# Kernel optimization log

Hardware: AMD Instinct MI355X
Metric: run time of the kernel (lower is better)

Reference implementation:

```python
import jax, jax.numpy as jnp
import numpy as np

EPS = 1e-5

# Binary activation with straight-through estimator (custom backward in the
# original torch.autograd.Function: grad scaled by 0.01 where |x| >= 1).
@jax.custom_vjp
def binact(x):
    return jnp.sign(x)

def _binact_fwd(x):
    return jnp.sign(x), x

def _binact_bwd(x, g):
    return (jnp.where((x >= 1.0) | (x <= -1.0), g * 0.01, g),)

binact.defvjp(_binact_fwd, _binact_bwd)


def batchnorm(x, gamma, beta):
    # training-mode BN: biased batch stats over (N, H, W)
    m = jnp.mean(x, axis=(0, 2, 3), keepdims=True)
    v = jnp.var(x, axis=(0, 2, 3), keepdims=True)
    return (x - m) * jax.lax.rsqrt(v + EPS) * gamma[None, :, None, None] + beta[None, :, None, None]


def prelu(x, alpha):
    return jnp.where(x >= 0, x, alpha[None, :, None, None] * x)


def binconv(x, w, stride):
    # per-output-channel scaling factor = mean |w| over (in, kh, kw), detached
    sf = jax.lax.stop_gradient(jnp.mean(jnp.abs(w), axis=(1, 2, 3), keepdims=True))
    bw = sf * jnp.sign(w)                       # binarized weight (+-sf)
    rc = jnp.clip(w, -1.0, 1.0)                 # STE path for gradients
    bf = jax.lax.stop_gradient(bw - rc) + rc    # forward=bw, backward=d(clip)
    return jax.lax.conv_general_dilated(
        x, bf, window_strides=(stride, stride), padding=[(1, 1), (1, 1)],
        dimension_numbers=("NCHW", "OIHW", "NCHW"))


def setup_inputs() -> dict:
    key = jax.random.key(0)
    ks = jax.random.split(key, 3)
    B, Cin, Cp, H = 32, 256, 256, 56
    x = jax.random.normal(ks[0], (B, Cin, H, H), jnp.float32)
    # original init: torch.rand(...) * 0.001; centered here so sign() has both polarities
    w1 = (jax.random.uniform(ks[1], (Cp, Cin, 3, 3), jnp.float32) * 2.0 - 1.0) * 0.001
    w2 = (jax.random.uniform(ks[2], (Cp, Cp, 3, 3), jnp.float32) * 2.0 - 1.0) * 0.001
    return {
        "x": x, "w1": w1, "w2": w2,
        "g1": jnp.ones((Cin,), jnp.float32), "b1": jnp.zeros((Cin,), jnp.float32),
        "g2": jnp.ones((Cp,), jnp.float32), "b2": jnp.zeros((Cp,), jnp.float32),
        "g3": jnp.ones((Cp,), jnp.float32), "b3": jnp.zeros((Cp,), jnp.float32),
        "a1": jnp.full((Cp,), 0.25, jnp.float32),
        "a2": jnp.full((Cp,), 0.25, jnp.float32),
        "a3": jnp.full((Cp,), 0.25, jnp.float32),
    }


def reference(x, w1, w2, g1, b1, g2, b2, g3, b3, a1, a2, a3):
    out = batchnorm(x, g1, b1)
    out = binact(out)
    out = prelu(binconv(out, w1, 1), a1)
    out = batchnorm(out, g2, b2)
    out = binact(out)
    out = binconv(out, w2, 1)
    out = prelu(out, a2)
    out = batchnorm(out, g3, b3)
    out = out + x  # identity shortcut (stride=1, in_planes == planes)
    return prelu(out, a3)
```

## Files before the change

kernel.cpp:

```cpp
#include <hip/hip_runtime.h>
#include <hip/hip_bf16.h>

typedef short short8 __attribute__((ext_vector_type(8)));
typedef float f32x4 __attribute__((ext_vector_type(4)));

#define NB 32
#define NC 256
#define HW 56
#define HALO 58
#define NPIX 100352
#define PIXB 3136

__device__ inline void gl_lds16(const void* g, void* l) {
    __builtin_amdgcn_global_load_lds(
        (const __attribute__((address_space(1))) void*)g,
        (__attribute__((address_space(3))) void*)l, 16, 0, 0);
}

__device__ inline unsigned short sgn_bf16(float v) {
    return v > 0.f ? (unsigned short)0x3F80 : (v < 0.f ? (unsigned short)0xBF80 : (unsigned short)0);
}

__global__ void halo_zero(unsigned short* __restrict__ s) {
    const uint4 z = {0u, 0u, 0u, 0u};
    const int total = 32 * 228 * 32;
    for (int v = blockIdx.x * 256 + threadIdx.x; v < total; v += gridDim.x * 256) {
        int cellg = v >> 5, q = v & 31;
        int b = cellg / 228;
        int cell = cellg - b * 228;
        int y, xx;
        if (cell < 58)       { y = 0;          xx = cell; }
        else if (cell < 116) { y = 57;         xx = cell - 58; }
        else if (cell < 172) { y = cell - 115; xx = 0; }
        else                 { y = cell - 171; xx = 57; }
        *(uint4*)(s + (((size_t)b * HALO + y) * HALO + xx) * 256 + q * 8) = z;
    }
}

__global__ void wprep_kernel(const float* __restrict__ w, unsigned short* __restrict__ wsgn,
                             float* __restrict__ sf) {
    int oc = blockIdx.x;
    const float* wp = w + (size_t)oc * 2304;
    unsigned short* op = wsgn + (size_t)oc * 2304;
    float s = 0.f;
    for (int idx = threadIdx.x; idx < 2304; idx += 256) {
        float v = wp[idx];
        s += fabsf(v);
        int ic = idx / 9;
        int k = idx - ic * 9;
        op[k * 256 + ic] = sgn_bf16(v);
    }
    #pragma unroll
    for (int m = 32; m; m >>= 1) s += __shfl_xor(s, m);
    __shared__ float rs[4];
    if ((threadIdx.x & 63) == 0) rs[threadIdx.x >> 6] = s;
    __syncthreads();
    if (threadIdx.x == 0) sf[oc] = (rs[0] + rs[1] + rs[2] + rs[3]) * (1.f / 2304.f);
}

__global__ void bn_stats_x(const float* __restrict__ x, double* __restrict__ ssum,
                           double* __restrict__ ssq) {
    int bid = blockIdx.x;
    int c = bid >> 3;
    int bg = bid & 7;
    float s = 0.f, q = 0.f;
    for (int b = bg * 4; b < bg * 4 + 4; ++b) {
        const float4* p = (const float4*)(x + ((size_t)(b * 256 + c)) * PIXB);
        for (int u = threadIdx.x; u < 784; u += 256) {
            float4 v = p[u];
            s += v.x + v.y + v.z + v.w;
            q += v.x * v.x + v.y * v.y + v.z * v.z + v.w * v.w;
        }
    }
    #pragma unroll
    for (int m = 32; m; m >>= 1) { s += __shfl_xor(s, m); q += __shfl_xor(q, m); }
    __shared__ float rs[4], rq[4];
    if ((threadIdx.x & 63) == 0) { rs[threadIdx.x >> 6] = s; rq[threadIdx.x >> 6] = q; }
    __syncthreads();
    if (threadIdx.x == 0) {
        atomicAdd(&ssum[c], (double)(rs[0] + rs[1] + rs[2] + rs[3]));
        atomicAdd(&ssq[c], (double)(rq[0] + rq[1] + rq[2] + rq[3]));
    }
}

__global__ void bn_finalize(const double* __restrict__ ssum, const double* __restrict__ ssq,
                            const float* __restrict__ g, const float* __restrict__ b,
                            float* __restrict__ scale, float* __restrict__ shift) {
    int c = threadIdx.x;
    double m = ssum[c] * (1.0 / (double)NPIX);
    double v = ssq[c] * (1.0 / (double)NPIX) - m * m;
    double sc = (double)g[c] / sqrt(v + 1e-5);
    scale[c] = (float)sc;
    shift[c] = (float)((double)b[c] - m * sc);
}

__global__ void sign1_kernel(const float* __restrict__ x, const float* __restrict__ scale,
                             const float* __restrict__ shift, unsigned short* __restrict__ sdst) {
    __shared__ unsigned short lds[64 * 57];
    int bid = blockIdx.x;
    int b = bid / 224;
    int rem = bid - b * 224;
    int h = rem >> 2;
    int cg = rem & 3;
    for (int idx = threadIdx.x; idx < 896; idx += 256) {
        int cl = idx / 14;
        int w4 = idx - cl * 14;
        int c = cg * 64 + cl;
        float4 v = *(const float4*)(x + ((((size_t)b * 256 + c) * 56 + h) * 56) + w4 * 4);
        float sc = scale[c], sh = shift[c];
        lds[cl * 57 + w4 * 4 + 0] = sgn_bf16(v.x * sc + sh);
        lds[cl * 57 + w4 * 4 + 1] = sgn_bf16(v.y * sc + sh);
        lds[cl * 57 + w4 * 4 + 2] = sgn_bf16(v.z * sc + sh);
        lds[cl * 57 + w4 * 4 + 3] = sgn_bf16(v.w * sc + sh);
    }
    __syncthreads();
    unsigned short* dst = sdst + (((size_t)b * HALO + h + 1) * HALO + 1) * 256 + cg * 64;
    for (int u = threadIdx.x; u < 896; u += 256) {
        int w = u >> 4;
        int c4 = u & 15;
        ushort4 o;
        o.x = lds[(c4 * 4 + 0) * 57 + w];
        o.y = lds[(c4 * 4 + 1) * 57 + w];
        o.z = lds[(c4 * 4 + 2) * 57 + w];
        o.w = lds[(c4 * 4 + 3) * 57 + w];
        *(ushort4*)(dst + w * 256 + c4 * 4) = o;
    }
}

__global__ void sign2_kernel(const float* __restrict__ y, const float* __restrict__ scale,
                             const float* __restrict__ shift, unsigned short* __restrict__ sdst) {
    int bid = blockIdx.x;
    int b = bid / 56;
    int h = bid - b * 56;
    const float4* src = (const float4*)(y + (size_t)bid * 56 * 256);
    unsigned short* dst = sdst + (((size_t)b * HALO + h + 1) * HALO + 1) * 256;
    for (int u = threadIdx.x; u < 3584; u += 256) {
        int c0 = (u & 63) * 4;
        float4 v = src[u];
        float4 sc = *(const float4*)(scale + c0);
        float4 sh = *(const float4*)(shift + c0);
        ushort4 o;
        o.x = sgn_bf16(v.x * sc.x + sh.x);
        o.y = sgn_bf16(v.y * sc.y + sh.y);
        o.z = sgn_bf16(v.z * sc.z + sh.z);
        o.w = sgn_bf16(v.w * sc.w + sh.w);
        *(ushort4*)(dst + (size_t)u * 4) = o;
    }
}

__global__ void conv_kernel(const unsigned short* __restrict__ sact,
                            const unsigned short* __restrict__ wsgn,
                            const float* __restrict__ sf, const float* __restrict__ alpha,
                            float* __restrict__ y, double* __restrict__ stat_sum,
                            double* __restrict__ stat_sumsq) {
    __shared__ char smem[16384];
    char* ldsA = smem;
    char* ldsB = smem + 8192;

    const int tid = threadIdx.x;
    const int lane = tid & 63;
    const int wave = tid >> 6;
    const int wm = wave >> 1, wn = wave & 1;

    const int bid = blockIdx.x;
    const int oc0 = (bid & 1) * 128;
    const int pix0 = (bid >> 1) * 128;

    const char* sBytes = (const char*)sact;
    const char* wBytes = (const char*)wsgn;
    int aBase[2], bBase[2];
    #pragma unroll
    for (int j = 0; j < 2; ++j) {
        int pix = pix0 + j * 64 + lane;
        int b = pix / PIXB;
        int rem = pix - b * PIXB;
        int oh = rem / 56;
        int ow = rem - oh * 56;
        aBase[j] = ((b * HALO + oh) * HALO + ow) * 512;
        bBase[j] = (oc0 + j * 64 + lane) * 4608;
    }

    f32x4 acc[4][4];
    #pragma unroll
    for (int m = 0; m < 4; ++m)
        #pragma unroll
        for (int n = 0; n < 4; ++n) acc[m][n] = {0.f, 0.f, 0.f, 0.f};

    const int fi = lane & 15;
    const int fc = lane >> 4;
    const int aOffBase = fc * 2048 + (wm * 64 + fi) * 16;
    const int bOffBase = fc * 2048 + (wn * 64 + fi) * 16;
    char* ldsA_st = ldsA + wave * 2048;
    char* ldsB_st = ldsB + wave * 2048;
    const int kSt = wave * 16;

    #pragma unroll 1
    for (int tap = 0; tap < 9; ++tap) {
        const int tapOff = ((tap / 3) * HALO + (tap % 3)) * 512;
        const int wTap = tap * 512;
        #pragma unroll
        for (int sl = 0; sl < 8; ++sl) {
            const int aoff = tapOff + sl * 64 + kSt;
            const int woff = wTap + sl * 64 + kSt;
            gl_lds16(sBytes + aBase[0] + aoff, ldsA_st);
            gl_lds16(sBytes + aBase[1] + aoff, ldsA_st + 1024);
            gl_lds16(wBytes + bBase[0] + woff, ldsB_st);
            gl_lds16(wBytes + bBase[1] + woff, ldsB_st + 1024);
            __syncthreads();
            short8 af[4], bf[4];
            #pragma unroll
            for (int m = 0; m < 4; ++m) af[m] = *(const short8*)(ldsA + aOffBase + m * 256);
            #pragma unroll
            for (int n = 0; n < 4; ++n) bf[n] = *(const short8*)(ldsB + bOffBase + n * 256);
            #pragma unroll
            for (int m = 0; m < 4; ++m)
                #pragma unroll
                for (int n = 0; n < 4; ++n)
                    acc[m][n] = __builtin_amdgcn_mfma_f32_16x16x32_bf16(af[m], bf[n], acc[m][n], 0, 0, 0);
            __syncthreads();
        }
    }

    float sfv[4], alv[4];
    #pragma unroll
    for (int n = 0; n < 4; ++n) {
        int oc = oc0 + wn * 64 + n * 16 + fi;
        sfv[n] = sf[oc];
        alv[n] = alpha[oc];
    }

    float* trans = (float*)smem;
    float* redS = (float*)(smem + 8192);
    float* redQ = (float*)(smem + 12288);
    const int cg = tid & 31;
    const int prw = tid >> 5;
    float ts[4] = {0.f, 0.f, 0.f, 0.f}, tq[4] = {0.f, 0.f, 0.f, 0.f};

    #pragma unroll
    for (int seg = 0; seg < 8; ++seg) {
        const int swm = seg >> 2, smi = seg & 3;
        if (wm == swm) {
            #pragma unroll
            for (int n = 0; n < 4; ++n) {
                f32x4 v = acc[smi][n];
                #pragma unroll
                for (int r = 0; r < 4; ++r) {
                    float val = v[r] * sfv[n];
                    val = val >= 0.f ? val : val * alv[n];
                    trans[(fc * 4 + r) * 128 + wn * 64 + n * 16 + fi] = val;
                }
            }
        }
        __syncthreads();
        #pragma unroll
        for (int i = 0; i < 2; ++i) {
            int p = prw + i * 8;
            f32x4 v = *(f32x4*)&trans[p * 128 + cg * 4];
            *(f32x4*)(y + (size_t)(pix0 + seg * 16 + p) * 256 + oc0 + cg * 4) = v;
            #pragma unroll
            for (int j = 0; j < 4; ++j) { ts[j] += v[j]; tq[j] += v[j] * v[j]; }
        }
        __syncthreads();
    }

    #pragma unroll
    for (int j = 0; j < 4; ++j) {
        redS[prw * 128 + cg * 4 + j] = ts[j];
        redQ[prw * 128 + cg * 4 + j] = tq[j];
    }
    __syncthreads();
    if (tid < 128) {
        float s = 0.f, q = 0.f;
        #pragma unroll
        for (int r = 0; r < 8; ++r) { s += redS[r * 128 + tid]; q += redQ[r * 128 + tid]; }
        atomicAdd(&stat_sum[oc0 + tid], (double)s);
        atomicAdd(&stat_sumsq[oc0 + tid], (double)q);
    }
}

__global__ void final_kernel(const float* __restrict__ z, const float* __restrict__ x,
                             const float* __restrict__ scale, const float* __restrict__ shift,
                             const float* __restrict__ a3, float* __restrict__ out) {
    __shared__ float lds[56 * 65];
    int bid = blockIdx.x;
    int b = bid / 224;
    int rem = bid - b * 224;
    int h = rem >> 2;
    int cg = rem & 3;
    for (int u = threadIdx.x; u < 896; u += 256) {
        int w = u >> 4;
        int c4 = u & 15;
        float4 v = *(const float4*)(z + ((size_t)(b * PIXB + h * 56 + w)) * 256 + cg * 64 + c4 * 4);
        int c = cg * 64 + c4 * 4;
        lds[w * 65 + c4 * 4 + 0] = v.x * scale[c + 0] + shift[c + 0];
        lds[w * 65 + c4 * 4 + 1] = v.y * scale[c + 1] + shift[c + 1];
        lds[w * 65 + c4 * 4 + 2] = v.z * scale[c + 2] + shift[c + 2];
        lds[w * 65 + c4 * 4 + 3] = v.w * scale[c + 3] + shift[c + 3];
    }
    __syncthreads();
    for (int u = threadIdx.x; u < 896; u += 256) {
        int cl = u / 14;
        int w4 = u - cl * 14;
        int c = cg * 64 + cl;
        size_t off = ((((size_t)b * 256 + c) * 56 + h) * 56) + w4 * 4;
        float4 xv = *(const float4*)(x + off);
        float av = a3[c];
        float4 o;
        o.x = lds[(w4 * 4 + 0) * 65 + cl] + xv.x;
        o.y = lds[(w4 * 4 + 1) * 65 + cl] + xv.y;
        o.z = lds[(w4 * 4 + 2) * 65 + cl] + xv.z;
        o.w = lds[(w4 * 4 + 3) * 65 + cl] + xv.w;
        o.x = o.x >= 0.f ? o.x : o.x * av;
        o.y = o.y >= 0.f ? o.y : o.y * av;
        o.z = o.z >= 0.f ? o.z : o.z * av;
        o.w = o.w >= 0.f ? o.w : o.w * av;
        *(float4*)(out + off) = o;
    }
}

extern "C" void kernel_launch(void* const* d_in, const int* in_sizes, int n_in,
                              void* d_out, int out_size, void* d_ws, size_t ws_size,
                              hipStream_t stream) {
    const float* x = (const float*)d_in[0];
    const float* w1 = (const float*)d_in[1];
    const float* w2 = (const float*)d_in[2];
    const float* g1 = (const float*)d_in[3];
    const float* b1 = (const float*)d_in[4];
    const float* g2 = (const float*)d_in[5];
    const float* b2 = (const float*)d_in[6];
    const float* g3 = (const float*)d_in[7];
    const float* b3 = (const float*)d_in[8];
    const float* a1 = (const float*)d_in[9];
    const float* a2 = (const float*)d_in[10];
    const float* a3 = (const float*)d_in[11];
    float* out = (float*)d_out;

    char* ws = (char*)d_ws;
    size_t off = 0;
    auto alloc = [&](size_t bytes) {
        char* p = ws + off;
        off += (bytes + 255) & ~(size_t)255;
        return p;
    };
    const size_t SBUF_BYTES = (size_t)NB * HALO * HALO * 256 * 2;
    unsigned short* s_buf = (unsigned short*)alloc(SBUF_BYTES);
    float* y_buf = (float*)alloc((size_t)NPIX * 256 * 4);
    unsigned short* wsg1 = (unsigned short*)alloc(256 * 2304 * 2);
    unsigned short* wsg2 = (unsigned short*)alloc(256 * 2304 * 2);
    float* sf1 = (float*)alloc(1024);
    float* sf2 = (float*)alloc(1024);
    double* stats = (double*)alloc(6 * 256 * 8);
    float* scales = (float*)alloc(6 * 256 * 4);

    double *sum1 = stats, *q1 = stats + 256, *sum2 = stats + 512, *q2 = stats + 768,
           *sum3 = stats + 1024, *q3 = stats + 1280;
    float *scale1 = scales, *shift1 = scales + 256, *scale2 = scales + 512,
          *shift2 = scales + 768, *scale3 = scales + 1024, *shift3 = scales + 1280;

    hipMemsetAsync(stats, 0, 6 * 256 * 8, stream);

    halo_zero<<<256, 256, 0, stream>>>(s_buf);
    wprep_kernel<<<256, 256, 0, stream>>>(w1, wsg1, sf1);
    wprep_kernel<<<256, 256, 0, stream>>>(w2, wsg2, sf2);
    bn_stats_x<<<2048, 256, 0, stream>>>(x, sum1, q1);
    bn_finalize<<<1, 256, 0, stream>>>(sum1, q1, g1, b1, scale1, shift1);
    sign1_kernel<<<7168, 256, 0, stream>>>(x, scale1, shift1, s_buf);
    conv_kernel<<<1568, 256, 0, stream>>>(s_buf, wsg1, sf1, a1, y_buf, sum2, q2);
    bn_finalize<<<1, 256, 0, stream>>>(sum2, q2, g2, b2, scale2, shift2);
    sign2_kernel<<<1792, 256, 0, stream>>>(y_buf, scale2, shift2, s_buf);
    conv_kernel<<<1568, 256, 0, stream>>>(s_buf, wsg2, sf2, a2, y_buf, sum3, q3);
    bn_finalize<<<1, 256, 0, stream>>>(sum3, q3, g3, b3, scale3, shift3);
    final_kernel<<<7168, 256, 0, stream>>>(y_buf, x, scale3, shift3, a3, out);
}
```

Measured before the change: 915.4 us.

## Double-buffer LDS staging in conv kernel and remap blocks across XCDs

The conv mainloop is flattened into 72 iterations with two LDS buffers, so the async global-to-LDS loads for the next K slice are issued before the MFMAs on the current slice. This overlaps memory latency with compute and needs only one barrier per iteration instead of two. The block index is also remapped (bid&7)*196+(bid>>3) so that neighbouring work tiles land on the same XCD, which should help L2 reuse. LDS use doubles to 32 KB, which may lower occupancy.

```diff
diff --git a/kernel.cpp b/kernel.cpp
--- a/kernel.cpp
+++ b/kernel.cpp
@@ -153,9 +153,7 @@
                             const float* __restrict__ sf, const float* __restrict__ alpha,
                             float* __restrict__ y, double* __restrict__ stat_sum,
                             double* __restrict__ stat_sumsq) {
-    __shared__ char smem[16384];
-    char* ldsA = smem;
-    char* ldsB = smem + 8192;
+    __shared__ char smem[32768];
 
     const int tid = threadIdx.x;
     const int lane = tid & 63;
@@ -163,8 +161,9 @@
     const int wm = wave >> 1, wn = wave & 1;
 
     const int bid = blockIdx.x;
-    const int oc0 = (bid & 1) * 128;
-    const int pix0 = (bid >> 1) * 128;
+    const int work = (bid & 7) * 196 + (bid >> 3);
+    const int oc0 = (work & 1) * 128;
+    const int pix0 = (work >> 1) * 128;
 
     const char* sBytes = (const char*)sact;
     const char* wBytes = (const char*)wsgn;
@@ -190,35 +189,42 @@
     const int fc = lane >> 4;
     const int aOffBase = fc * 2048 + (wm * 64 + fi) * 16;
     const int bOffBase = fc * 2048 + (wn * 64 + fi) * 16;
-    char* ldsA_st = ldsA + wave * 2048;
-    char* ldsB_st = ldsB + wave * 2048;
+    const int stA = wave * 2048;
     const int kSt = wave * 16;
 
+    auto STAGE = [&](int it, int c) {
+        int tap = it >> 3, sl = it & 7;
+        int ty = tap / 3, tx = tap - ty * 3;
+        int aoff = (ty * HALO + tx) * 512 + sl * 64 + kSt;
+        int woff = tap * 512 + sl * 64 + kSt;
+        char* dstA = smem + c * 16384 + stA;
+        char* dstB = smem + c * 16384 + 8192 + stA;
+        gl_lds16(sBytes + aBase[0] + aoff, dstA);
+        gl_lds16(sBytes + aBase[1] + aoff, dstA + 1024);
+        gl_lds16(wBytes + bBase[0] + woff, dstB);
+        gl_lds16(wBytes + bBase[1] + woff, dstB + 1024);
+    };
+
+    STAGE(0, 0);
+    __syncthreads();
+    int cur = 0;
     #pragma unroll 1
-    for (int tap = 0; tap < 9; ++tap) {
-        const int tapOff = ((tap / 3) * HALO + (tap % 3)) * 512;
-        const int wTap = tap * 512;
-        #pragma unroll
-        for (int sl = 0; sl < 8; ++sl) {
-            const int aoff = tapOff + sl * 64 + kSt;
-            const int woff = wTap + sl * 64 + kSt;
-            gl_lds16(sBytes + aBase[0] + aoff, ldsA_st);
-            gl_lds16(sBytes + aBase[1] + aoff, ldsA_st + 1024);
-            gl_lds16(wBytes + bBase[0] + woff, ldsB_st);
-            gl_lds16(wBytes + bBase[1] + woff, ldsB_st + 1024);
-            __syncthreads();
-            short8 af[4], bf[4];
+    for (int it = 0; it < 72; ++it) {
+        if (it < 71) STAGE(it + 1, cur ^ 1);
+        const char* rdA = smem + cur * 16384;
+        const char* rdB = rdA + 8192;
+        short8 af[4], bf[4];
+        #pragma unroll
+        for (int m = 0; m < 4; ++m) af[m] = *(const short8*)(rdA + aOffBase + m * 256);
+        #pragma unroll
+        for (int n = 0; n < 4; ++n) bf[n] = *(const short8*)(rdB + bOffBase + n * 256);
+        #pragma unroll
+        for (int m = 0; m < 4; ++m)
             #pragma unroll
-            for (int m = 0; m < 4; ++m) af[m] = *(const short8*)(ldsA + aOffBase + m * 256);
-            #pragma unroll
-            for (int n = 0; n < 4; ++n) bf[n] = *(const short8*)(ldsB + bOffBase + n * 256);
-            #pragma unroll
-            for (int m = 0; m < 4; ++m)
-                #pragma unroll
-                for (int n = 0; n < 4; ++n)
-                    acc[m][n] = __builtin_amdgcn_mfma_f32_16x16x32_bf16(af[m], bf[n], acc[m][n], 0, 0, 0);
-            __syncthreads();
-        }
+            for (int n = 0; n < 4; ++n)
+                acc[m][n] = __builtin_amdgcn_mfma_f32_16x16x32_bf16(af[m], bf[n], acc[m][n], 0, 0, 0);
+        __syncthreads();
+        cur ^= 1;
     }
 
     float sfv[4], alv[4];
```

Result: no change. 900.7 us (-1.6%).
